# Performance work log

Hardware: AMD Instinct MI355X
Metric: run time of the kernel (lower is better)

The kernel has to match this reference:

```python
import jax, jax.numpy as jnp
import numpy as np

N_NODES = 50000
N_EDGES = 600000
IN_FEAT = 128
OUT_FEAT = 128
NUM_RELS = 8


def setup_inputs() -> dict:
    key = jax.random.key(0)
    ks = jax.random.split(key, 8)
    h = jax.random.normal(ks[0], (N_NODES, IN_FEAT), dtype=jnp.float32)
    # xavier_uniform-like scale for relation weights
    limit = float(np.sqrt(6.0 / (IN_FEAT + OUT_FEAT)))
    weight = jax.random.uniform(ks[1], (NUM_RELS, IN_FEAT, OUT_FEAT), jnp.float32, -limit, limit)
    limit_g = float(np.sqrt(6.0 / (IN_FEAT + 1)))
    gate_weight = jax.random.uniform(ks[2], (NUM_RELS, IN_FEAT, 1), jnp.float32, -limit_g, limit_g)
    h_bias = jnp.zeros((OUT_FEAT,), jnp.float32)
    loop_weight = jax.random.uniform(ks[3], (IN_FEAT, OUT_FEAT), jnp.float32, -limit, limit)
    norm = jax.random.uniform(ks[4], (N_EDGES, 1), jnp.float32)
    src = jax.random.randint(ks[5], (N_EDGES,), 0, N_NODES, dtype=jnp.int32)
    dst = jax.random.randint(ks[6], (N_EDGES,), 0, N_NODES, dtype=jnp.int32)
    rel_type = jax.random.randint(ks[7], (N_EDGES,), 0, NUM_RELS, dtype=jnp.int32)
    return {"h": h, "weight": weight, "gate_weight": gate_weight, "h_bias": h_bias,
            "loop_weight": loop_weight, "norm": norm, "src": src, "dst": dst,
            "rel_type": rel_type}


def reference(h, weight, gate_weight, h_bias, loop_weight, norm, src, dst, rel_type):
    n_nodes = h.shape[0]
    # Transform all nodes under every relation once ([R, N, out]); cheaper than
    # materializing per-edge [E, in, out] weight gathers for small R.
    h_rel = jnp.einsum('ni,rio->rno', h, weight)          # [R, N, out]
    msg = h_rel[rel_type, src]                             # [E, out] gather
    msg = msg * norm                                       # per-edge norm
    # relation-specific scalar gate on src features
    gate_rel = jnp.einsum('ni,ri->rn', h, gate_weight[:, :, 0])  # [R, N]
    gate = jax.nn.sigmoid(gate_rel[rel_type, src])[:, None]      # [E, 1]
    msg = msg * gate
    # scatter-sum messages into destination nodes
    agg = jax.ops.segment_sum(msg, dst, num_segments=n_nodes)    # [N, out]
    out = agg + h_bias + h @ loop_weight                   # bias + self-loop
    out = jax.nn.relu(out)                                 # activation
    # dropout p=0.0 (deterministic) -> identity
    return out
```

## Files before the change

### kernel.cpp

```cpp
#include <hip/hip_runtime.h>

#define N_NODES 50000
#define N_EDGES 600000
#define F 128
#define NRELL 9
#define NB_SCAN 196
#define NB2 1563

#define WT3_OFF   0
#define H2_OFF    294912
#define GATE3_OFF 13094912
#define CNT3_OFF  14694912
#define EXCL3_OFF 16294912
#define BSUM3_OFF 17895168
#define REC3_OFF  17901568
#define A3_OFF    22701568
#define WS_NEED3  ((size_t)125199872)

#define GATE_OFF   294912
#define HREL_OFF   1894912
#define HREL_BYTES (9ll*N_NODES*128*2)
#define CNT_OFF    117094912
#define BASE_OFF   117294912
#define CUR_OFF    117494912
#define BSUM_OFF   117694912
#define SORT_OFF   117695936
#define WS_NEED2   ((size_t)120095936)
#define WS_NEED1   ((size_t)HREL_OFF + (size_t)HREL_BYTES)

typedef __attribute__((ext_vector_type(8))) short short8;
typedef __attribute__((ext_vector_type(4))) float floatx4;

__device__ inline unsigned short f32_to_bf16(float f) {
    unsigned u = __float_as_uint(f);
    unsigned r = u + 0x7fff + ((u >> 16) & 1);
    return (unsigned short)(r >> 16);
}
__device__ inline float bf16_to_f32(unsigned short s) {
    return __uint_as_float(((unsigned)s) << 16);
}
__device__ inline float bf16lo(unsigned m) { return __uint_as_float(m << 16); }
__device__ inline float bf16hi(unsigned m) { return __uint_as_float(m & 0xffff0000u); }
__device__ inline float sigmoidf(float x) { return 1.f / (1.f + __expf(-x)); }
__device__ inline unsigned packbf(float a0, float a1) {
    return (unsigned)f32_to_bf16(a0) | ((unsigned)f32_to_bf16(a1) << 16);
}

__device__ __forceinline__ void gload_lds16(const void* gsrc, void* ldst) {
    __builtin_amdgcn_global_load_lds(
        (const __attribute__((address_space(1))) void*)gsrc,
        (__attribute__((address_space(3))) void*)ldst, 16, 0, 0);
}

__global__ __launch_bounds__(256) void k_prep(
    const float* __restrict__ h, const float* __restrict__ W,
    const float* __restrict__ gw, const float* __restrict__ lw,
    const int* __restrict__ dst, const int* __restrict__ rel,
    unsigned short* __restrict__ Wt, unsigned short* __restrict__ h2,
    float* __restrict__ gate, int* __restrict__ cnt)
{
    int vb = blockIdx.x, tid = threadIdx.x;
    if (vb < 576) {
        int idx = vb * 256 + tid;
        int r = idx >> 14, rem = idx & 16383, i = rem >> 7, o = rem & 127;
        float v = (r < 8) ? W[(r << 14) + (i << 7) + o] : lw[(i << 7) + o];
        int g = (i >> 3) ^ (o & 7);
        Wt[(r << 14) + (o << 7) + (g << 3) + (i & 7)] = f32_to_bf16(v);
    } else if (vb < 6826) {
        int idx = (vb - 576) * 1024 + tid * 4;
        float4 v = *(const float4*)(h + idx);
        ushort4 b;
        b.x = f32_to_bf16(v.x); b.y = f32_to_bf16(v.y);
        b.z = f32_to_bf16(v.z); b.w = f32_to_bf16(v.w);
        *(ushort4*)(h2 + idx) = b;
    } else if (vb < 7608) {
        int wave = tid >> 6, lane = tid & 63;
        int wid = (vb - 6826) * 4 + wave;
        int n0 = wid * 16;
        int rl = lane >> 3, seg = lane & 7;
        const float4* wp = (const float4*)(gw + rl * F + seg * 16);
        float4 w0 = wp[0], w1 = wp[1], w2 = wp[2], w3 = wp[3];
        #pragma unroll 4
        for (int i = 0; i < 16; ++i) {
            int n = n0 + i;
            if (n >= N_NODES) break;
            const float4* hp = (const float4*)(h + (size_t)n * F + seg * 16);
            float4 a0 = hp[0], a1 = hp[1], a2 = hp[2], a3 = hp[3];
            float p = a0.x * w0.x + a0.y * w0.y + a0.z * w0.z + a0.w * w0.w;
            p += a1.x * w1.x + a1.y * w1.y + a1.z * w1.z + a1.w * w1.w;
            p += a2.x * w2.x + a2.y * w2.y + a2.z * w2.z + a2.w * w2.w;
            p += a3.x * w3.x + a3.y * w3.y + a3.z * w3.z + a3.w * w3.w;
            p += __shfl_xor(p, 1);
            p += __shfl_xor(p, 2);
            p += __shfl_xor(p, 4);
            if (seg == 0) gate[(size_t)n * 8 + rl] = sigmoidf(p);
        }
    } else {
        int e = (vb - 7608) * 256 + tid;
        if (e < N_EDGES) atomicAdd(&cnt[dst[e] * 8 + rel[e]], 1);
    }
}

__global__ void k_s1(const int* __restrict__ cnt, int* __restrict__ excl,
                     int* __restrict__ bsum) {
    __shared__ int sh[256];
    int g = blockIdx.x * 256 + threadIdx.x;
    int v = (g < 400000) ? cnt[g] : 0;
    sh[threadIdx.x] = v;
    __syncthreads();
    #pragma unroll
    for (int off = 1; off < 256; off <<= 1) {
        int t = (threadIdx.x >= off) ? sh[threadIdx.x - off] : 0;
        __syncthreads();
        sh[threadIdx.x] += t;
        __syncthreads();
    }
    if (g < 400000) excl[g] = sh[threadIdx.x] - v;
    if (threadIdx.x == 255) bsum[blockIdx.x] = sh[255];
}

__global__ void k_s2(int* __restrict__ bsum) {
    __shared__ int sh[256];
    int t = threadIdx.x;
    int v[7];
    int s = 0;
    #pragma unroll
    for (int j = 0; j < 7; ++j) {
        int idx = t * 7 + j;
        v[j] = (idx < NB2) ? bsum[idx] : 0;
        s += v[j];
    }
    sh[t] = s;
    __syncthreads();
    #pragma unroll
    for (int off = 1; off < 256; off <<= 1) {
        int tt = (t >= off) ? sh[t - off] : 0;
        __syncthreads();
        sh[t] += tt;
        __syncthreads();
    }
    int run = sh[t] - s;
    #pragma unroll
    for (int j = 0; j < 7; ++j) {
        int idx = t * 7 + j;
        if (idx < NB2) bsum[idx] = run;
        run += v[j];
    }
}

__global__ void k_s3(int* __restrict__ excl, const int* __restrict__ bsum,
                     int* __restrict__ cursor) {
    int g = blockIdx.x * 256 + threadIdx.x;
    if (g < 400000) {
        int b = excl[g] + bsum[blockIdx.x];
        excl[g] = b;
        cursor[g] = b;
    }
    if (g == 0) excl[400000] = N_EDGES;
}

__global__ void k_scatter2(const int* __restrict__ src, const int* __restrict__ dst,
                           const int* __restrict__ rel, const float* __restrict__ norm,
                           const float* __restrict__ gate, int* __restrict__ cursor,
                           int2* __restrict__ rec) {
    int e = blockIdx.x * 256 + threadIdx.x;
    if (e >= N_EDGES) return;
    int d = dst[e], r = rel[e], s = src[e];
    int pos = atomicAdd(&cursor[d * 8 + r], 1);
    float sc = norm[e] * gate[(size_t)s * 8 + r];
    rec[pos] = make_int2(s, __float_as_int(sc));
}

__global__ __launch_bounds__(256) void k_aggA(const unsigned short* __restrict__ h2,
                                              const int2* __restrict__ rec,
                                              const int* __restrict__ excl,
                                              unsigned short* __restrict__ A) {
    int wave = threadIdx.x >> 6, lane = threadIdx.x & 63;
    int n = blockIdx.x * 4 + wave;
    int ex = 0;
    if (lane < 9) ex = excl[n * 8 + lane];
    int e0 = __shfl(ex, 0), e8 = __shfl(ex, 8);
    int deg = e8 - e0;
    unsigned short* Arow = A + (size_t)n * 1024;
    int swo = (((lane >> 2) ^ (n & 7)) << 2) + (lane & 3);

    if (deg <= 64) {
        int rs = 0; float rsc = 0.f;
        if (lane < deg) {
            int2 rc = rec[e0 + lane];
            rs = rc.x; rsc = __int_as_float(rc.y);
        }
        for (int r = 0; r < 8; ++r) {
            int s = __shfl(ex, r) - e0;
            int e = __shfl(ex, r + 1) - e0;
            float a0 = 0.f, a1 = 0.f;
            for (int j = s; j < e; ++j) {
                int sj = __shfl(rs, j);
                float sc = __shfl(rsc, j);
                unsigned m = *(const unsigned*)(h2 + (size_t)sj * F + lane * 2);
                a0 += sc * bf16lo(m);
                a1 += sc * bf16hi(m);
            }
            ((unsigned*)(Arow + r * 128))[swo] = packbf(a0, a1);
        }
    } else {
        for (int r = 0; r < 8; ++r) {
            int s = __shfl(ex, r);
            int e = __shfl(ex, r + 1);
            float a0 = 0.f, a1 = 0.f;
            for (int idx = s; idx < e; ++idx) {
                int2 rc = rec[idx];
                float sc = __int_as_float(rc.y);
                unsigned m = *(const unsigned*)(h2 + (size_t)rc.x * F + lane * 2);
                a0 += sc * bf16lo(m);
                a1 += sc * bf16hi(m);
            }
            ((unsigned*)(Arow + r * 128))[swo] = packbf(a0, a1);
        }
    }
}

__global__ __launch_bounds__(256) void k_gemmA(const unsigned short* __restrict__ A,
                                               const unsigned short* __restrict__ h2,
                                               const unsigned short* __restrict__ Wt,
                                               const float* __restrict__ bias,
                                               float* __restrict__ out) {
    __shared__ unsigned short sB[16384];
    int tid = threadIdx.x;
    int nb = blockIdx.x * 64;
    int wave = tid >> 6, lane = tid & 63, lrow = lane & 15, quad = lane >> 4;
    int wr = wave >> 1, wc = wave & 1;

    floatx4 acc[2][4];
    #pragma unroll
    for (int mt = 0; mt < 2; ++mt)
        #pragma unroll
        for (int nt = 0; nt < 4; ++nt) acc[mt][nt] = (floatx4){0.f, 0.f, 0.f, 0.f};

    const unsigned short* Ar0 = A + (size_t)(nb + wr * 32 + lrow) * 1024;
    const unsigned short* Ar1 = Ar0 + (size_t)16 * 1024;
    const unsigned short* Hr0 = h2 + (size_t)(nb + wr * 32 + lrow) * F;
    const unsigned short* Hr1 = Hr0 + (size_t)16 * F;
    int sk = lrow & 7;

    for (int kb = 0; kb < 9; ++kb) {
        short8 a0r[4], a1r[4];
        if (kb < 8) {
            #pragma unroll
            for (int kt = 0; kt < 4; ++kt) {
                int gphys = ((kt * 4 + quad) ^ sk) << 3;
                a0r[kt] = *(const short8*)(Ar0 + kb * 128 + gphys);
                a1r[kt] = *(const short8*)(Ar1 + kb * 128 + gphys);
            }
        } else {
            #pragma unroll
            for (int kt = 0; kt < 4; ++kt) {
                int goff = (kt * 4 + quad) << 3;
                a0r[kt] = *(const short8*)(Hr0 + goff);
                a1r[kt] = *(const short8*)(Hr1 + goff);
            }
        }
        __syncthreads();
        #pragma unroll
        for (int it = 0; it < 8; ++it) {
            int c = it * 4 + wave;
            gload_lds16((const char*)Wt + (kb << 15) + (c << 10) + lane * 16,
                        (char*)sB + (c << 10));
        }
        __syncthreads();
        #pragma unroll
        for (int kt = 0; kt < 4; ++kt) {
            int gphys = ((kt * 4 + quad) ^ sk) << 3;
            #pragma unroll
            for (int nt = 0; nt < 4; ++nt) {
                short8 b = *(const short8*)(&sB[(wc * 64 + nt * 16 + lrow) * 128 + gphys]);
                acc[0][nt] = __builtin_amdgcn_mfma_f32_16x16x32_bf16(a0r[kt], b, acc[0][nt], 0, 0, 0);
                acc[1][nt] = __builtin_amdgcn_mfma_f32_16x16x32_bf16(a1r[kt], b, acc[1][nt], 0, 0, 0);
            }
        }
    }
    #pragma unroll
    for (int mt = 0; mt < 2; ++mt) {
        #pragma unroll
        for (int nt = 0; nt < 4; ++nt) {
            int col = wc * 64 + nt * 16 + lrow;
            float bv = bias[col];
            #pragma unroll
            for (int g = 0; g < 4; ++g) {
                int row = nb + wr * 32 + mt * 16 + quad * 4 + g;
                if (row < N_NODES)
                    out[(size_t)row * F + col] = fmaxf(acc[mt][nt][g] + bv, 0.f);
            }
        }
    }
}

__global__ void k_prep_w(const float* __restrict__ W, const float* __restrict__ LW,
                         unsigned short* __restrict__ Wt, int swz) {
    int idx = blockIdx.x * 256 + threadIdx.x;
    if (idx >= 9 * 128 * 128) return;
    int r = idx >> 14;
    int rem = idx & 16383;
    int i = rem >> 7, o = rem & 127;
    float v = (r < 8) ? W[(r << 14) + (i << 7) + o] : LW[(i << 7) + o];
    int pos;
    if (swz) {
        int g = (i >> 3) ^ (o & 7);
        pos = (r << 14) + (o << 7) + (g << 3) + (i & 7);
    } else {
        pos = (r << 14) + (o << 7) + i;
    }
    Wt[pos] = f32_to_bf16(v);
}

__global__ void k_gate(const float* __restrict__ h, const float* __restrict__ gw,
                       float* __restrict__ gate) {
    int wave = threadIdx.x >> 6, lane = threadIdx.x & 63;
    int n = blockIdx.x * 4 + wave;
    if (n >= N_NODES) return;
    float2 hv = *(const float2*)(h + (size_t)n * F + lane * 2);
    #pragma unroll
    for (int r = 0; r < 8; ++r) {
        float2 wv = *(const float2*)(gw + r * F + lane * 2);
        float p = hv.x * wv.x + hv.y * wv.y;
        #pragma unroll
        for (int off = 32; off; off >>= 1) p += __shfl_xor(p, off);
        if (lane == 0) gate[r * N_NODES + n] = sigmoidf(p);
    }
}

#define LDH 136
#define LDW 136
__global__ __launch_bounds__(256) void k_hrel(const float* __restrict__ h,
                                              const unsigned short* __restrict__ Wt,
                                              unsigned short* __restrict__ hrel) {
    __shared__ unsigned short hA[64 * LDH];
    __shared__ unsigned short wB[128 * LDW];
    int tid = threadIdx.x;
    int nb = blockIdx.x * 64;
    #pragma unroll
    for (int it = 0; it < 8; ++it) {
        int idx = it * 1024 + tid * 4;
        int row = idx >> 7, col = idx & 127;
        int node = nb + row;
        float4 v;
        if (node < N_NODES) v = *(const float4*)(h + (size_t)node * F + col);
        else                v = make_float4(0.f, 0.f, 0.f, 0.f);
        ushort4 b;
        b.x = f32_to_bf16(v.x); b.y = f32_to_bf16(v.y);
        b.z = f32_to_bf16(v.z); b.w = f32_to_bf16(v.w);
        *(ushort4*)(&hA[row * LDH + col]) = b;
    }
    int wave = tid >> 6, lane = tid & 63;
    int lrow = lane & 15, quad = lane >> 4;
    const unsigned short* aptr = &hA[(wave * 16 + lrow) * LDH + quad * 8];
    for (int r = 0; r < NRELL; ++r) {
        __syncthreads();
        #pragma unroll
        for (int it = 0; it < 8; ++it) {
            int idx = it * 2048 + tid * 8;
            int o = idx >> 7, i = idx & 127;
            *(uint4*)(&wB[o * LDW + i]) = *(const uint4*)(Wt + (r << 14) + idx);
        }
        __syncthreads();
        floatx4 acc[8];
        #pragma unroll
        for (int nt = 0; nt < 8; ++nt) acc[nt] = (floatx4){0.f, 0.f, 0.f, 0.f};
        #pragma unroll
        for (int kt = 0; kt < 4; ++kt) {
            short8 a = *(const short8*)(aptr + kt * 32);
            #pragma unroll
            for (int nt = 0; nt < 8; ++nt) {
                short8 b = *(const short8*)(&wB[(nt * 16 + lrow) * LDW + kt * 32 + quad * 8]);
                acc[nt] = __builtin_amdgcn_mfma_f32_16x16x32_bf16(a, b, acc[nt], 0, 0, 0);
            }
        }
        unsigned short* dstp = hrel + (size_t)r * N_NODES * F;
        #pragma unroll
        for (int nt = 0; nt < 8; ++nt) {
            #pragma unroll
            for (int g = 0; g < 4; ++g) {
                int node = nb + wave * 16 + quad * 4 + g;
                if (node < N_NODES)
                    dstp[(size_t)node * F + nt * 16 + lrow] = f32_to_bf16(acc[nt][g]);
            }
        }
    }
}

__global__ void k_hist(const int* __restrict__ dst, int* __restrict__ cnt) {
    int e = blockIdx.x * 256 + threadIdx.x;
    if (e < N_EDGES) atomicAdd(&cnt[dst[e]], 1);
}

__global__ void k_scan1(const int* __restrict__ cnt, int* __restrict__ excl,
                        int* __restrict__ bsum) {
    __shared__ int sh[256];
    int g = blockIdx.x * 256 + threadIdx.x;
    int v = (g < N_NODES) ? cnt[g] : 0;
    sh[threadIdx.x] = v;
    __syncthreads();
    #pragma unroll
    for (int off = 1; off < 256; off <<= 1) {
        int t = (threadIdx.x >= off) ? sh[threadIdx.x - off] : 0;
        __syncthreads();
        sh[threadIdx.x] += t;
        __syncthreads();
    }
    if (g < N_NODES) excl[g] = sh[threadIdx.x] - v;
    if (threadIdx.x == 255) bsum[blockIdx.x] = sh[255];
}

__global__ void k_scan2(int* __restrict__ bsum) {
    __shared__ int sh[256];
    int v = (threadIdx.x < NB_SCAN) ? bsum[threadIdx.x] : 0;
    sh[threadIdx.x] = v;
    __syncthreads();
    #pragma unroll
    for (int off = 1; off < 256; off <<= 1) {
        int t = (threadIdx.x >= off) ? sh[threadIdx.x - off] : 0;
        __syncthreads();
        sh[threadIdx.x] += t;
        __syncthreads();
    }
    if (threadIdx.x < NB_SCAN) bsum[threadIdx.x] = sh[threadIdx.x] - v;
}

__global__ void k_scan3(int* __restrict__ excl, const int* __restrict__ bsum,
                        int* __restrict__ cursor) {
    int g = blockIdx.x * 256 + threadIdx.x;
    if (g < N_NODES) {
        int b = excl[g] + bsum[blockIdx.x];
        excl[g] = b;
        cursor[g] = b;
    }
}

__global__ void k_scatter(const int* __restrict__ dst, int* __restrict__ cursor,
                          int* __restrict__ sorted) {
    int e = blockIdx.x * 256 + threadIdx.x;
    if (e < N_EDGES) {
        int pos = atomicAdd(&cursor[dst[e]], 1);
        sorted[pos] = e;
    }
}

__global__ __launch_bounds__(256) void k_agg(const unsigned short* __restrict__ hrel,
                      const float* __restrict__ gate,
                      const float* __restrict__ norm,
                      const int* __restrict__ src, const int* __restrict__ rel,
                      const int* __restrict__ sorted,
                      const int* __restrict__ base, const int* __restrict__ cnt,
                      const float* __restrict__ bias,
                      float* __restrict__ out) {
    int wave = threadIdx.x >> 6, lane = threadIdx.x & 63;
    int n = blockIdx.x * 4 + wave;
    if (n >= N_NODES) return;
    int startp = base[n];
    int deg = cnt[n];
    float acc0 = 0.f, acc1 = 0.f;
    for (int c0 = 0; c0 < deg; c0 += 64) {
        int myi = c0 + lane;
        float sc = 0.f;
        int row = 0;
        if (myi < deg) {
            int e = sorted[startp + myi];
            int s = src[e], r = rel[e];
            row = r * N_NODES + s;
            sc = norm[e] * gate[row];
        }
        int lim = (deg - c0 < 64) ? (deg - c0) : 64;
        for (int i = 0; i < lim; ++i) {
            float scl = __shfl(sc, i);
            int rw = __shfl(row, i);
            unsigned m = *(const unsigned*)(hrel + (size_t)rw * F + lane * 2);
            acc0 += scl * bf16lo(m);
            acc1 += scl * bf16hi(m);
        }
    }
    const unsigned short* hrel8 = hrel + (size_t)8 * N_NODES * F;
    unsigned l8 = *(const unsigned*)(hrel8 + (size_t)n * F + lane * 2);
    float2 bv = *(const float2*)(bias + lane * 2);
    float o0 = fmaxf(acc0 + bv.x + bf16lo(l8), 0.f);
    float o1 = fmaxf(acc1 + bv.y + bf16hi(l8), 0.f);
    *(float2*)(out + (size_t)n * F + lane * 2) = make_float2(o0, o1);
}

__global__ void k_edges(const unsigned short* __restrict__ hrel,
                        const float* __restrict__ gate,
                        const float* __restrict__ norm,
                        const int* __restrict__ src, const int* __restrict__ dst,
                        const int* __restrict__ rel,
                        float* __restrict__ out) {
    int wave = threadIdx.x >> 6, lane = threadIdx.x & 63;
    int e = blockIdx.x * 4 + wave;
    if (e >= N_EDGES) return;
    int s = src[e], d = dst[e], r = rel[e];
    float scale = norm[e] * gate[r * N_NODES + s];
    unsigned int m = *(const unsigned int*)(hrel + ((size_t)r * N_NODES + s) * F + lane * 2);
    float v0 = bf16lo(m) * scale;
    float v1 = bf16hi(m) * scale;
    float* op = out + (size_t)d * F + lane * 2;
    unsafeAtomicAdd(op, v0);
    unsafeAtomicAdd(op + 1, v1);
}

__global__ void k_final(float* __restrict__ out, const float* __restrict__ bias,
                        const unsigned short* __restrict__ hrel8) {
    int idx = blockIdx.x * 256 + threadIdx.x;
    if (idx >= N_NODES * 32) return;
    int node = idx >> 5, c4 = (idx & 31) * 4;
    float4 a = *(float4*)(out + (size_t)node * F + c4);
    float4 b = *(const float4*)(bias + c4);
    ushort4 l = *(const ushort4*)(hrel8 + (size_t)node * F + c4);
    float o0 = fmaxf(a.x + b.x + bf16_to_f32(l.x), 0.f);
    float o1 = fmaxf(a.y + b.y + bf16_to_f32(l.y), 0.f);
    float o2 = fmaxf(a.z + b.z + bf16_to_f32(l.z), 0.f);
    float o3 = fmaxf(a.w + b.w + bf16_to_f32(l.w), 0.f);
    *(float4*)(out + (size_t)node * F + c4) = make_float4(o0, o1, o2, o3);
}

__global__ void k_edges_fb(const float* __restrict__ h, const float* __restrict__ W,
                           const float* __restrict__ gw, const float* __restrict__ norm,
                           const int* __restrict__ src, const int* __restrict__ dst,
                           const int* __restrict__ rel, float* __restrict__ out) {
    int wave = threadIdx.x >> 6, lane = threadIdx.x & 63;
    int e = blockIdx.x * 4 + wave;
    if (e >= N_EDGES) return;
    int s = src[e], d = dst[e], r = rel[e];
    float2 hv = *(const float2*)(h + (size_t)s * F + lane * 2);
    float2 gv = *(const float2*)(gw + r * F + lane * 2);
    float p = hv.x * gv.x + hv.y * gv.y;
    #pragma unroll
    for (int off = 32; off; off >>= 1) p += __shfl_xor(p, off);
    float scale = norm[e] * sigmoidf(p);
    const float* wr = W + ((size_t)r << 14);
    float a0 = 0.f, a1 = 0.f;
    for (int i2 = 0; i2 < 64; ++i2) {
        float x0 = __shfl(hv.x, i2), x1 = __shfl(hv.y, i2);
        a0 += x0 * wr[(2 * i2) * F + lane]      + x1 * wr[(2 * i2 + 1) * F + lane];
        a1 += x0 * wr[(2 * i2) * F + 64 + lane] + x1 * wr[(2 * i2 + 1) * F + 64 + lane];
    }
    unsafeAtomicAdd(out + (size_t)d * F + lane,      a0 * scale);
    unsafeAtomicAdd(out + (size_t)d * F + 64 + lane, a1 * scale);
}

__global__ void k_final_fb(const float* __restrict__ h, const float* __restrict__ LW,
                           const float* __restrict__ bias, float* __restrict__ out) {
    int wave = threadIdx.x >> 6, lane = threadIdx.x & 63;
    int n = blockIdx.x * 4 + wave;
    if (n >= N_NODES) return;
    float2 hv = *(const float2*)(h + (size_t)n * F + lane * 2);
    float a0 = 0.f, a1 = 0.f;
    for (int i2 = 0; i2 < 64; ++i2) {
        float x0 = __shfl(hv.x, i2), x1 = __shfl(hv.y, i2);
        a0 += x0 * LW[(2 * i2) * F + lane]      + x1 * LW[(2 * i2 + 1) * F + lane];
        a1 += x0 * LW[(2 * i2) * F + 64 + lane] + x1 * LW[(2 * i2 + 1) * F + 64 + lane];
    }
    float* op = out + (size_t)n * F;
    op[lane]      = fmaxf(op[lane]      + bias[lane]      + a0, 0.f);
    op[64 + lane] = fmaxf(op[64 + lane] + bias[64 + lane] + a1, 0.f);
}

extern "C" void kernel_launch(void* const* d_in, const int* in_sizes, int n_in,
                              void* d_out, int out_size, void* d_ws, size_t ws_size,
                              hipStream_t stream) {
    const float* h    = (const float*)d_in[0];
    const float* W    = (const float*)d_in[1];
    const float* gw   = (const float*)d_in[2];
    const float* bias = (const float*)d_in[3];
    const float* lw   = (const float*)d_in[4];
    const float* norm = (const float*)d_in[5];
    const int* src    = (const int*)d_in[6];
    const int* dst    = (const int*)d_in[7];
    const int* rel    = (const int*)d_in[8];
    float* out = (float*)d_out;

    if (ws_size >= WS_NEED3) {
        unsigned short* Wt   = (unsigned short*)((char*)d_ws + WT3_OFF);
        unsigned short* h2   = (unsigned short*)((char*)d_ws + H2_OFF);
        float*          gate = (float*)((char*)d_ws + GATE3_OFF);
        int*            cnt  = (int*)((char*)d_ws + CNT3_OFF);
        int*            excl = (int*)((char*)d_ws + EXCL3_OFF);
        int*            bsum = (int*)((char*)d_ws + BSUM3_OFF);
        int2*           rec  = (int2*)((char*)d_ws + REC3_OFF);
        unsigned short* A    = (unsigned short*)((char*)d_ws + A3_OFF);

        hipMemsetAsync(cnt, 0, 400000 * sizeof(int), stream);
        k_prep<<<9952, 256, 0, stream>>>(h, W, gw, lw, dst, rel, Wt, h2, gate, cnt);
        k_s1<<<NB2, 256, 0, stream>>>(cnt, excl, bsum);
        k_s2<<<1, 256, 0, stream>>>(bsum);
        k_s3<<<NB2, 256, 0, stream>>>(excl, bsum, cnt);
        k_scatter2<<<2344, 256, 0, stream>>>(src, dst, rel, norm, gate, cnt, rec);
        k_aggA<<<12500, 256, 0, stream>>>(h2, rec, excl, A);
        k_gemmA<<<782, 256, 0, stream>>>(A, h2, Wt, bias, out);
    } else if (ws_size >= WS_NEED2) {
        unsigned short* Wt   = (unsigned short*)d_ws;
        float*          gate = (float*)((char*)d_ws + GATE_OFF);
        unsigned short* hrel = (unsigned short*)((char*)d_ws + HREL_OFF);
        int* cnt    = (int*)((char*)d_ws + CNT_OFF);
        int* base   = (int*)((char*)d_ws + BASE_OFF);
        int* cursor = (int*)((char*)d_ws + CUR_OFF);
        int* bsum   = (int*)((char*)d_ws + BSUM_OFF);
        int* sorted = (int*)((char*)d_ws + SORT_OFF);
        hipMemsetAsync(cnt, 0, N_NODES * sizeof(int), stream);
        k_prep_w<<<576, 256, 0, stream>>>(W, lw, Wt, 0);
        k_gate<<<12500, 256, 0, stream>>>(h, gw, gate);
        k_hist<<<2344, 256, 0, stream>>>(dst, cnt);
        k_scan1<<<NB_SCAN, 256, 0, stream>>>(cnt, base, bsum);
        k_scan2<<<1, 256, 0, stream>>>(bsum);
        k_scan3<<<NB_SCAN, 256, 0, stream>>>(base, bsum, cursor);
        k_scatter<<<2344, 256, 0, stream>>>(dst, cursor, sorted);
        k_hrel<<<782, 256, 0, stream>>>(h, Wt, hrel);
        k_agg<<<12500, 256, 0, stream>>>(hrel, gate, norm, src, rel, sorted,
                                         base, cnt, bias, out);
    } else if (ws_size >= WS_NEED1) {
        unsigned short* Wt   = (unsigned short*)d_ws;
        float*          gate = (float*)((char*)d_ws + GATE_OFF);
        unsigned short* hrel = (unsigned short*)((char*)d_ws + HREL_OFF);
        hipMemsetAsync(d_out, 0, (size_t)out_size * sizeof(float), stream);
        k_prep_w<<<576, 256, 0, stream>>>(W, lw, Wt, 0);
        k_gate<<<12500, 256, 0, stream>>>(h, gw, gate);
        k_hrel<<<782, 256, 0, stream>>>(h, Wt, hrel);
        k_edges<<<150000, 256, 0, stream>>>(hrel, gate, norm, src, dst, rel, out);
        k_final<<<6250, 256, 0, stream>>>(out, bias, hrel + (size_t)8 * N_NODES * F);
    } else {
        hipMemsetAsync(d_out, 0, (size_t)out_size * sizeof(float), stream);
        k_edges_fb<<<150000, 256, 0, stream>>>(h, W, gw, norm, src, dst, rel, out);
        k_final_fb<<<12500, 256, 0, stream>>>(h, lw, bias, out);
    }
}
```

Before: 259.0 us.

## Fuse per-relation aggregation and GEMM into one kernel via shared memory

Replaces the separate aggregation kernel, which wrote a bf16 [N,8*128] intermediate to global memory, and the GEMM kernel that read it back, with a single fused kernel. Each 512-thread block gathers 32 nodes' per-relation sums plus their self features into shared memory, then runs MFMA against the weights read directly from global memory. This removes roughly 100 MB of intermediate write and read traffic and one launch, and lowers the workspace requirement. In exchange, B tiles are no longer staged in LDS, and the large shared-memory footprint limits occupancy during the latency-bound gather phase.

Measured after the change: 287.3 us. 1.11x slower.

```diff
diff --git a/kernel.cpp b/kernel.cpp
--- a/kernel.cpp
+++ b/kernel.cpp
@@ -14,8 +14,7 @@
 #define EXCL3_OFF 16294912
 #define BSUM3_OFF 17895168
 #define REC3_OFF  17901568
-#define A3_OFF    22701568
-#define WS_NEED3  ((size_t)125199872)
+#define WS_NEED3  ((size_t)22701568)
 
 #define GATE_OFF   294912
 #define HREL_OFF   1894912
@@ -28,6 +27,9 @@
 #define WS_NEED2   ((size_t)120095936)
 #define WS_NEED1   ((size_t)HREL_OFF + (size_t)HREL_BYTES)
 
+#define FBN 32
+#define FGRID 1563
+
 typedef __attribute__((ext_vector_type(8))) short short8;
 typedef __attribute__((ext_vector_type(4))) float floatx4;
 
@@ -44,12 +46,6 @@
 __device__ inline float sigmoidf(float x) { return 1.f / (1.f + __expf(-x)); }
 __device__ inline unsigned packbf(float a0, float a1) {
     return (unsigned)f32_to_bf16(a0) | ((unsigned)f32_to_bf16(a1) << 16);
-}
-
-__device__ __forceinline__ void gload_lds16(const void* gsrc, void* ldst) {
-    __builtin_amdgcn_global_load_lds(
-        (const __attribute__((address_space(1))) void*)gsrc,
-        (__attribute__((address_space(3))) void*)ldst, 16, 0, 0);
 }
 
 __global__ __launch_bounds__(256) void k_prep(
@@ -171,127 +167,95 @@
     rec[pos] = make_int2(s, __float_as_int(sc));
 }
 
-__global__ __launch_bounds__(256) void k_aggA(const unsigned short* __restrict__ h2,
-                                              const int2* __restrict__ rec,
-                                              const int* __restrict__ excl,
-                                              unsigned short* __restrict__ A) {
-    int wave = threadIdx.x >> 6, lane = threadIdx.x & 63;
-    int n = blockIdx.x * 4 + wave;
-    int ex = 0;
-    if (lane < 9) ex = excl[n * 8 + lane];
-    int e0 = __shfl(ex, 0), e8 = __shfl(ex, 8);
-    int deg = e8 - e0;
-    unsigned short* Arow = A + (size_t)n * 1024;
-    int swo = (((lane >> 2) ^ (n & 7)) << 2) + (lane & 3);
-
-    if (deg <= 64) {
-        int rs = 0; float rsc = 0.f;
-        if (lane < deg) {
-            int2 rc = rec[e0 + lane];
-            rs = rc.x; rsc = __int_as_float(rc.y);
-        }
-        for (int r = 0; r < 8; ++r) {
-            int s = __shfl(ex, r) - e0;
-            int e = __shfl(ex, r + 1) - e0;
-            float a0 = 0.f, a1 = 0.f;
-            for (int j = s; j < e; ++j) {
-                int sj = __shfl(rs, j);
-                float sc = __shfl(rsc, j);
-                unsigned m = *(const unsigned*)(h2 + (size_t)sj * F + lane * 2);
-                a0 += sc * bf16lo(m);
-                a1 += sc * bf16hi(m);
+__global__ __launch_bounds__(512, 4) void k_fused(
+    const unsigned short* __restrict__ h2,
+    const int2* __restrict__ rec,
+    const int* __restrict__ excl,
+    const unsigned short* __restrict__ Wt,
+    const float* __restrict__ bias,
+    float* __restrict__ out)
+{
+    __shared__ unsigned short sA[FBN * 1152];
+    unsigned* sAu = (unsigned*)sA;
+    int tid = threadIdx.x;
+    int wave = tid >> 6, lane = tid & 63;
+    int nb = blockIdx.x * FBN;
+
+    #pragma unroll
+    for (int i = 0; i < 4; ++i) {
+        int n = nb + wave * 4 + i;
+        int lr = wave * 4 + i;
+        int bin = n * 8 + lane;
+        int ex = 0;
+        if (lane < 9) ex = excl[bin <= 400000 ? bin : 400000];
+        int e0 = __shfl(ex, 0), e8 = __shfl(ex, 8);
+        int deg = e8 - e0;
+        unsigned* aw = sAu + lr * 576 + (((lane >> 2) ^ (lr & 7)) << 2) + (lane & 3);
+
+        if (deg <= 64) {
+            int rs = 0; float rsc = 0.f;
+            if (lane < deg) {
+                int2 rc = rec[e0 + lane];
+                rs = rc.x; rsc = __int_as_float(rc.y);
             }
-            ((unsigned*)(Arow + r * 128))[swo] = packbf(a0, a1);
-        }
-    } else {
-        for (int r = 0; r < 8; ++r) {
-            int s = __shfl(ex, r);
-            int e = __shfl(ex, r + 1);
-            float a0 = 0.f, a1 = 0.f;
-            for (int idx = s; idx < e; ++idx) {
-                int2 rc = rec[idx];
-                float sc = __int_as_float(rc.y);
-                unsigned m = *(const unsigned*)(h2 + (size_t)rc.x * F + lane * 2);
-                a0 += sc * bf16lo(m);
-                a1 += sc * bf16hi(m);
-            }
-            ((unsigned*)(Arow + r * 128))[swo] = packbf(a0, a1);
-        }
-    }
-}
-
-__global__ __launch_bounds__(256) void k_gemmA(const unsigned short* __restrict__ A,
-                                               const unsigned short* __restrict__ h2,
-                                               const unsigned short* __restrict__ Wt,
-                                               const float* __restrict__ bias,
-                                               float* __restrict__ out) {
-    __shared__ unsigned short sB[16384];
-    int tid = threadIdx.x;
-    int nb = blockIdx.x * 64;
-    int wave = tid >> 6, lane = tid & 63, lrow = lane & 15, quad = lane >> 4;
-    int wr = wave >> 1, wc = wave & 1;
-
-    floatx4 acc[2][4];
-    #pragma unroll
-    for (int mt = 0; mt < 2; ++mt)
-        #pragma unroll
-        for (int nt = 0; nt < 4; ++nt) acc[mt][nt] = (floatx4){0.f, 0.f, 0.f, 0.f};
-
-    const unsigned short* Ar0 = A + (size_t)(nb + wr * 32 + lrow) * 1024;
-    const unsigned short* Ar1 = Ar0 + (size_t)16 * 1024;
-    const unsigned short* Hr0 = h2 + (size_t)(nb + wr * 32 + lrow) * F;
-    const unsigned short* Hr1 = Hr0 + (size_t)16 * F;
-    int sk = lrow & 7;
-
-    for (int kb = 0; kb < 9; ++kb) {
-        short8 a0r[4], a1r[4];
-        if (kb < 8) {
-            #pragma unroll
-            for (int kt = 0; kt < 4; ++kt) {
-                int gphys = ((kt * 4 + quad) ^ sk) << 3;
-                a0r[kt] = *(const short8*)(Ar0 + kb * 128 + gphys);
-                a1r[kt] = *(const short8*)(Ar1 + kb * 128 + gphys);
+            for (int r = 0; r < 8; ++r) {
+                int s = __shfl(ex, r) - e0;
+                int e = __shfl(ex, r + 1) - e0;
+                float a0 = 0.f, a1 = 0.f;
+                for (int j = s; j < e; ++j) {
+                    int sj = __shfl(rs, j);
+                    float sc = __shfl(rsc, j);
+                    unsigned m = *(const unsigned*)(h2 + (size_t)sj * F + lane * 2);
+                    a0 += sc * bf16lo(m);
+                    a1 += sc * bf16hi(m);
+                }
+                aw[r * 64] = packbf(a0, a1);
             }
         } else {
-            #pragma unroll
-            for (int kt = 0; kt < 4; ++kt) {
-                int goff = (kt * 4 + quad) << 3;
-                a0r[kt] = *(const short8*)(Hr0 + goff);
-                a1r[kt] = *(const short8*)(Hr1 + goff);
+            for (int r = 0; r < 8; ++r) {
+                int s = __shfl(ex, r);
+                int e = __shfl(ex, r + 1);
+                float a0 = 0.f, a1 = 0.f;
+                for (int idx = s; idx < e; ++idx) {
+                    int2 rc = rec[idx];
+                    float sc = __int_as_float(rc.y);
+                    unsigned m = *(const unsigned*)(h2 + (size_t)rc.x * F + lane * 2);
+                    a0 += sc * bf16lo(m);
+                    a1 += sc * bf16hi(m);
+                }
+                aw[r * 64] = packbf(a0, a1);
             }
         }
-        __syncthreads();
-        #pragma unroll
-        for (int it = 0; it < 8; ++it) {
-            int c = it * 4 + wave;
-            gload_lds16((const char*)Wt + (kb << 15) + (c << 10) + lane * 16,
-                        (char*)sB + (c << 10));
-        }
-        __syncthreads();
+        unsigned hm = 0;
+        if (n < N_NODES) hm = ((const unsigned*)(h2 + (size_t)n * F))[lane];
+        aw[512] = hm;
+    }
+    __syncthreads();
+
+    int lrow = lane & 15, quad = lane >> 4;
+    int sk = lrow & 7;
+    const unsigned short* Bcol = Wt + ((wave * 16 + lrow) << 7);
+    floatx4 acc0 = (floatx4){0.f, 0.f, 0.f, 0.f};
+    floatx4 acc1 = (floatx4){0.f, 0.f, 0.f, 0.f};
+    for (int r = 0; r < 9; ++r) {
         #pragma unroll
         for (int kt = 0; kt < 4; ++kt) {
             int gphys = ((kt * 4 + quad) ^ sk) << 3;
-            #pragma unroll
-            for (int nt = 0; nt < 4; ++nt) {
-                short8 b = *(const short8*)(&sB[(wc * 64 + nt * 16 + lrow) * 128 + gphys]);
-                acc[0][nt] = __builtin_amdgcn_mfma_f32_16x16x32_bf16(a0r[kt], b, acc[0][nt], 0, 0, 0);
-                acc[1][nt] = __builtin_amdgcn_mfma_f32_16x16x32_bf16(a1r[kt], b, acc[1][nt], 0, 0, 0);
-            }
-        }
-    }
-    #pragma unroll
-    for (int mt = 0; mt < 2; ++mt) {
-        #pragma unroll
-        for (int nt = 0; nt < 4; ++nt) {
-            int col = wc * 64 + nt * 16 + lrow;
-            float bv = bias[col];
-            #pragma unroll
-            for (int g = 0; g < 4; ++g) {
-                int row = nb + wr * 32 + mt * 16 + quad * 4 + g;
-                if (row < N_NODES)
-                    out[(size_t)row * F + col] = fmaxf(acc[mt][nt][g] + bv, 0.f);
-            }
-        }
+            short8 b  = *(const short8*)(Bcol + (r << 14) + gphys);
+            short8 a0 = *(const short8*)(&sA[lrow * 1152 + r * 128 + gphys]);
+            short8 a1 = *(const short8*)(&sA[(16 + lrow) * 1152 + r * 128 + gphys]);
+            acc0 = __builtin_amdgcn_mfma_f32_16x16x32_bf16(a0, b, acc0, 0, 0, 0);
+            acc1 = __builtin_amdgcn_mfma_f32_16x16x32_bf16(a1, b, acc1, 0, 0, 0);
+        }
+    }
+    int col = wave * 16 + lrow;
+    float bv = bias[col];
+    #pragma unroll
+    for (int g = 0; g < 4; ++g) {
+        int row0 = nb + quad * 4 + g;
+        if (row0 < N_NODES) out[(size_t)row0 * F + col] = fmaxf(acc0[g] + bv, 0.f);
+        int row1 = nb + 16 + quad * 4 + g;
+        if (row1 < N_NODES) out[(size_t)row1 * F + col] = fmaxf(acc1[g] + bv, 0.f);
     }
 }
 
@@ -584,7 +548,6 @@
         int*            excl = (int*)((char*)d_ws + EXCL3_OFF);
         int*            bsum = (int*)((char*)d_ws + BSUM3_OFF);
         int2*           rec  = (int2*)((char*)d_ws + REC3_OFF);
-        unsigned short* A    = (unsigned short*)((char*)d_ws + A3_OFF);
 
         hipMemsetAsync(cnt, 0, 400000 * sizeof(int), stream);
         k_prep<<<9952, 256, 0, stream>>>(h, W, gw, lw, dst, rel, Wt, h2, gate, cnt);
@@ -592,8 +555,7 @@
         k_s2<<<1, 256, 0, stream>>>(bsum);
         k_s3<<<NB2, 256, 0, stream>>>(excl, bsum, cnt);
         k_scatter2<<<2344, 256, 0, stream>>>(src, dst, rel, norm, gate, cnt, rec);
-        k_aggA<<<12500, 256, 0, stream>>>(h2, rec, excl, A);
-        k_gemmA<<<782, 256, 0, stream>>>(A, h2, Wt, bias, out);
+        k_fused<<<FGRID, 512, 0, stream>>>(h2, rec, excl, Wt, bias, out);
     } else if (ws_size >= WS_NEED2) {
         unsigned short* Wt   = (unsigned short*)d_ws;
         float*          gate = (float*)((char*)d_ws + GATE_OFF);
```
